# Kernel tuning notes

Measured on AMD Instinct MI355X. Metric: run time of the kernel, lower is better.

The kernel has to match this reference:

```python
import jax, jax.numpy as jnp
import numpy as np

B, IN_F, OUT_F = 1024, 256, 256
GRID_SIZE, K = 5, 3  # grid_size, spline_order
N_BASIS = GRID_SIZE + K


def _make_grid():
    h = (1.0 - (-1.0)) / GRID_SIZE
    return jnp.linspace(-1.0 - K * h, 1.0 + K * h, GRID_SIZE + 2 * K + 1, dtype=jnp.float32)


def compute_bspline_basis(x, grid, k):
    # x: (N,), grid: (G + 2k + 1,) -> (N, G + k)
    x = x[:, None]
    bases = ((x >= grid[:-1]) & (x < grid[1:])).astype(x.dtype)
    for p in range(1, k + 1):
        n = bases.shape[1] - 1
        left_den = jnp.clip(grid[p:p + n] - grid[:n], 1e-8)
        left = (x - grid[:n]) / left_den * bases[:, :n]
        right_den = jnp.clip(grid[p + 1:p + 1 + n] - grid[1:1 + n], 1e-8)
        right = (grid[p + 1:p + 1 + n] - x) / right_den * bases[:, 1:1 + n]
        bases = left + right
    # boundary fix: x at/above last interior knot falls into last basis
    bases = bases.at[:, -1].add((x[:, 0] >= grid[-k - 1]).astype(x.dtype))
    return bases


def setup_inputs() -> dict:
    key = jax.random.key(0)
    kx, kc, kb = jax.random.split(key, 3)
    x = jax.random.normal(kx, (B, IN_F), dtype=jnp.float32)
    coeff = jax.random.normal(kc, (OUT_F, IN_F, N_BASIS), dtype=jnp.float32) / np.sqrt(IN_F * N_BASIS)
    base_weight = jax.random.normal(kb, (OUT_F, IN_F), dtype=jnp.float32) / np.sqrt(IN_F)
    spline_weight = jnp.ones((OUT_F, IN_F), dtype=jnp.float32)
    grid = _make_grid()
    return {"x": x, "grid": grid, "coeff": coeff,
            "base_weight": base_weight, "spline_weight": spline_weight}


def reference(x, grid, coeff, base_weight, spline_weight):
    batch = x.shape[0]
    bases = compute_bspline_basis(x.reshape(-1), grid, K)          # (B*in, n_basis)
    bases = bases.reshape(batch, IN_F, N_BASIS)                     # (b, i, n)
    spline_out = jnp.einsum('bin,oin->boi', bases, coeff)           # (b, o, i)
    spline_out = spline_out * spline_weight[None, :, :]
    base_out = jax.nn.silu(x)[:, None, :] * base_weight[None, :, :]  # (b, o, i)
    return (spline_out + base_out).sum(axis=2)                      # (b, o)
```

## Files before the change

### kernel.cpp

```cpp
#include <hip/hip_runtime.h>
#include <hip/hip_bf16.h>

#define B_SZ   1024
#define IN_F   256
#define OUT_F  256
#define NB     9
#define KTOT   (IN_F * NB)
#define NGRID  12

typedef __attribute__((ext_vector_type(8))) short  bf16x8;
typedef __attribute__((ext_vector_type(16))) float f32x16;

__global__ __launch_bounds__(256) void kan_prep(
    const float* __restrict__ x,
    const float* __restrict__ grid,
    const float* __restrict__ coeff,
    const float* __restrict__ bw,
    const float* __restrict__ sw,
    __hip_bfloat16* __restrict__ phi,
    __hip_bfloat16* __restrict__ W) {
  if (blockIdx.x < (B_SZ * IN_F) / 256) {
    int idx = blockIdx.x * 256 + threadIdx.x;
    float g[NGRID];
#pragma unroll
    for (int j = 0; j < NGRID; ++j) g[j] = grid[j];
    float xv = x[idx];

    float bas[NGRID - 1];
#pragma unroll
    for (int j = 0; j < NGRID - 1; ++j)
      bas[j] = (xv >= g[j] && xv < g[j + 1]) ? 1.0f : 0.0f;

    float h = g[1] - g[0];
    float r1 = __builtin_amdgcn_rcpf(h);
    float rp[3] = { r1, 0.5f * r1, (1.0f / 3.0f) * r1 };

#pragma unroll
    for (int p = 1; p <= 3; ++p) {
      int n = NGRID - 1 - p;
      float inv = rp[p - 1];
#pragma unroll
      for (int j = 0; j < n; ++j) {
        bas[j] = ((xv - g[j]) * bas[j] + (g[p + 1 + j] - xv) * bas[j + 1]) * inv;
      }
    }
    bas[7] += (xv >= g[NGRID - 4]) ? 1.0f : 0.0f;
    float sil = xv / (1.0f + __expf(-xv));

    int b = idx >> 8;
    int i = idx & 255;
    __hip_bfloat16* dst = phi + (size_t)b * KTOT + i;
#pragma unroll
    for (int n = 0; n < 8; ++n) dst[n * IN_F] = __float2bfloat16(bas[n]);
    dst[8 * IN_F] = __float2bfloat16(sil);
  } else {
    int idx = (blockIdx.x - (B_SZ * IN_F) / 256) * 256 + threadIdx.x;
    int o = idx >> 8;
    int i = idx & 255;
    float s = sw[idx];
    const float4* c4 = (const float4*)(coeff + (size_t)idx * 8);
    float4 c0 = c4[0];
    float4 c1 = c4[1];
    __hip_bfloat16* dst = W + (size_t)o * KTOT + i;
    dst[0 * IN_F] = __float2bfloat16(s * c0.x);
    dst[1 * IN_F] = __float2bfloat16(s * c0.y);
    dst[2 * IN_F] = __float2bfloat16(s * c0.z);
    dst[3 * IN_F] = __float2bfloat16(s * c0.w);
    dst[4 * IN_F] = __float2bfloat16(s * c1.x);
    dst[5 * IN_F] = __float2bfloat16(s * c1.y);
    dst[6 * IN_F] = __float2bfloat16(s * c1.z);
    dst[7 * IN_F] = __float2bfloat16(s * c1.w);
    dst[8 * IN_F] = __float2bfloat16(bw[idx]);
  }
}

#define KSEG (KTOT / 16)

__global__ __launch_bounds__(1024) void kan_gemm(
    const __hip_bfloat16* __restrict__ phi,
    const __hip_bfloat16* __restrict__ W,
    float* __restrict__ out) {
  __shared__ float partial[8][32 * 32];

  int tid  = threadIdx.x;
  int wave = tid >> 6;
  int lane = tid & 63;
  int bm = (blockIdx.x & 31) * 32;
  int bn = (blockIdx.x >> 5) * 32;
  int r = lane & 31;
  int h = lane >> 5;

  const short* ap = (const short*)(phi + (size_t)(bm + r) * KTOT) + wave * KSEG + h * 8;
  const short* bp = (const short*)(W   + (size_t)(bn + r) * KTOT) + wave * KSEG + h * 8;

  f32x16 acc;
#pragma unroll
  for (int g = 0; g < 16; ++g) acc[g] = 0.0f;

#pragma unroll 3
  for (int k = 0; k < KSEG; k += 16) {
    bf16x8 a = *(const bf16x8*)(ap + k);
    bf16x8 b = *(const bf16x8*)(bp + k);
    acc = __builtin_amdgcn_mfma_f32_32x32x16_bf16(a, b, acc, 0, 0, 0);
  }

  float* pw = &partial[wave & 7][0];
  if (wave < 8) {
#pragma unroll
    for (int g = 0; g < 16; ++g) {
      int row = (g & 3) + 8 * (g >> 2) + 4 * h;
      pw[row * 32 + r] = acc[g];
    }
  }
  __syncthreads();
  if (wave >= 8) {
#pragma unroll
    for (int g = 0; g < 16; ++g) {
      int row = (g & 3) + 8 * (g >> 2) + 4 * h;
      pw[row * 32 + r] += acc[g];
    }
  }
  __syncthreads();

  float s = 0.0f;
#pragma unroll
  for (int w = 0; w < 8; ++w) s += partial[w][tid];
  int row = tid >> 5, col = tid & 31;
  out[(size_t)(bm + row) * OUT_F + bn + col] = s;
}

extern "C" void kernel_launch(void* const* d_in, const int* in_sizes, int n_in,
                              void* d_out, int out_size, void* d_ws, size_t ws_size,
                              hipStream_t stream) {
  const float* x     = (const float*)d_in[0];
  const float* grid  = (const float*)d_in[1];
  const float* coeff = (const float*)d_in[2];
  const float* bw    = (const float*)d_in[3];
  const float* sw    = (const float*)d_in[4];
  float* out = (float*)d_out;

  __hip_bfloat16* phi = (__hip_bfloat16*)d_ws;
  __hip_bfloat16* W   = phi + (size_t)B_SZ * KTOT;

  kan_prep<<<(B_SZ * IN_F + OUT_F * IN_F) / 256, 256, 0, stream>>>(
      x, grid, coeff, bw, sw, phi, W);
  kan_gemm<<<(B_SZ / 32) * (OUT_F / 32), 1024, 0, stream>>>(phi, W, out);
}
```

Baseline: 75.35 us.

## Fuse basis/weight preparation into GEMM kernel using LDS-staged tiles

Merges the prep and GEMM kernels into one launch. Each block computes B-spline bases and SiLU for its 32 batch rows and the scaled bf16 weights for its 32 outputs directly into shared memory, in two K-chunks, then runs MFMA over them with 12 waves. This removes the global workspace round trip and the second launch. In exchange, basis and weight work is recomputed redundantly across blocks, and LDS stores with a stride of 9 may cause bank conflicts.

Result: slower. 82.04 us (+8.9%).

```diff
diff --git a/kernel.cpp b/kernel.cpp
--- a/kernel.cpp
+++ b/kernel.cpp
@@ -8,125 +8,137 @@
 #define KTOT   (IN_F * NB)
 #define NGRID  12
 
+#define ICH    128
+#define KCH    (ICH * NB)
+#define STR    (KCH + 8)
+#define NWAVE  12
+#define THREADS 768
+#define KSEG   (KCH / NWAVE)
+
 typedef __attribute__((ext_vector_type(8))) short  bf16x8;
 typedef __attribute__((ext_vector_type(16))) float f32x16;
 
-__global__ __launch_bounds__(256) void kan_prep(
+__device__ __forceinline__ short f2bs(float v) {
+  __hip_bfloat16 b = __float2bfloat16(v);
+  return *reinterpret_cast<short*>(&b);
+}
+
+__global__ __launch_bounds__(THREADS) void kan_fused(
     const float* __restrict__ x,
     const float* __restrict__ grid,
     const float* __restrict__ coeff,
     const float* __restrict__ bw,
     const float* __restrict__ sw,
-    __hip_bfloat16* __restrict__ phi,
-    __hip_bfloat16* __restrict__ W) {
-  if (blockIdx.x < (B_SZ * IN_F) / 256) {
-    int idx = blockIdx.x * 256 + threadIdx.x;
-    float g[NGRID];
-#pragma unroll
-    for (int j = 0; j < NGRID; ++j) g[j] = grid[j];
-    float xv = x[idx];
-
-    float bas[NGRID - 1];
-#pragma unroll
-    for (int j = 0; j < NGRID - 1; ++j)
-      bas[j] = (xv >= g[j] && xv < g[j + 1]) ? 1.0f : 0.0f;
-
-    float h = g[1] - g[0];
-    float r1 = __builtin_amdgcn_rcpf(h);
-    float rp[3] = { r1, 0.5f * r1, (1.0f / 3.0f) * r1 };
-
-#pragma unroll
-    for (int p = 1; p <= 3; ++p) {
-      int n = NGRID - 1 - p;
-      float inv = rp[p - 1];
-#pragma unroll
-      for (int j = 0; j < n; ++j) {
-        bas[j] = ((xv - g[j]) * bas[j] + (g[p + 1 + j] - xv) * bas[j + 1]) * inv;
-      }
-    }
-    bas[7] += (xv >= g[NGRID - 4]) ? 1.0f : 0.0f;
-    float sil = xv / (1.0f + __expf(-xv));
-
-    int b = idx >> 8;
-    int i = idx & 255;
-    __hip_bfloat16* dst = phi + (size_t)b * KTOT + i;
-#pragma unroll
-    for (int n = 0; n < 8; ++n) dst[n * IN_F] = __float2bfloat16(bas[n]);
-    dst[8 * IN_F] = __float2bfloat16(sil);
-  } else {
-    int idx = (blockIdx.x - (B_SZ * IN_F) / 256) * 256 + threadIdx.x;
-    int o = idx >> 8;
-    int i = idx & 255;
-    float s = sw[idx];
-    const float4* c4 = (const float4*)(coeff + (size_t)idx * 8);
-    float4 c0 = c4[0];
-    float4 c1 = c4[1];
-    __hip_bfloat16* dst = W + (size_t)o * KTOT + i;
-    dst[0 * IN_F] = __float2bfloat16(s * c0.x);
-    dst[1 * IN_F] = __float2bfloat16(s * c0.y);
-    dst[2 * IN_F] = __float2bfloat16(s * c0.z);
-    dst[3 * IN_F] = __float2bfloat16(s * c0.w);
-    dst[4 * IN_F] = __float2bfloat16(s * c1.x);
-    dst[5 * IN_F] = __float2bfloat16(s * c1.y);
-    dst[6 * IN_F] = __float2bfloat16(s * c1.z);
-    dst[7 * IN_F] = __float2bfloat16(s * c1.w);
-    dst[8 * IN_F] = __float2bfloat16(bw[idx]);
-  }
-}
-
-#define KSEG (KTOT / 16)
-
-__global__ __launch_bounds__(1024) void kan_gemm(
-    const __hip_bfloat16* __restrict__ phi,
-    const __hip_bfloat16* __restrict__ W,
     float* __restrict__ out) {
-  __shared__ float partial[8][32 * 32];
+  __shared__ __align__(16) short smem[2 * 32 * STR];
+  short* As = smem;
+  short* Bs = smem + 32 * STR;
 
   int tid  = threadIdx.x;
   int wave = tid >> 6;
   int lane = tid & 63;
+  int r = lane & 31;
+  int h = lane >> 5;
   int bm = (blockIdx.x & 31) * 32;
   int bn = (blockIdx.x >> 5) * 32;
-  int r = lane & 31;
-  int h = lane >> 5;
 
-  const short* ap = (const short*)(phi + (size_t)(bm + r) * KTOT) + wave * KSEG + h * 8;
-  const short* bp = (const short*)(W   + (size_t)(bn + r) * KTOT) + wave * KSEG + h * 8;
+  float g[NGRID];
+#pragma unroll
+  for (int j = 0; j < NGRID; ++j) g[j] = grid[j];
+  float hh = g[1] - g[0];
+  float r1 = __builtin_amdgcn_rcpf(hh);
+  float rp[3] = { r1, 0.5f * r1, (1.0f / 3.0f) * r1 };
 
   f32x16 acc;
 #pragma unroll
-  for (int g = 0; g < 16; ++g) acc[g] = 0.0f;
+  for (int q = 0; q < 16; ++q) acc[q] = 0.0f;
 
-#pragma unroll 3
-  for (int k = 0; k < KSEG; k += 16) {
-    bf16x8 a = *(const bf16x8*)(ap + k);
-    bf16x8 b = *(const bf16x8*)(bp + k);
-    acc = __builtin_amdgcn_mfma_f32_32x32x16_bf16(a, b, acc, 0, 0, 0);
+  for (int c = 0; c < 2; ++c) {
+    int i0 = c * ICH;
+
+    for (int p = tid; p < 32 * ICH; p += THREADS) {
+      int row = p >> 7;
+      int i   = p & (ICH - 1);
+      float xv = x[(size_t)(bm + row) * IN_F + i0 + i];
+
+      float bas[NGRID - 1];
+#pragma unroll
+      for (int j = 0; j < NGRID - 1; ++j)
+        bas[j] = (xv >= g[j] && xv < g[j + 1]) ? 1.0f : 0.0f;
+#pragma unroll
+      for (int p3 = 1; p3 <= 3; ++p3) {
+        int n = NGRID - 1 - p3;
+        float inv = rp[p3 - 1];
+#pragma unroll
+        for (int j = 0; j < n; ++j)
+          bas[j] = ((xv - g[j]) * bas[j] + (g[p3 + 1 + j] - xv) * bas[j + 1]) * inv;
+      }
+      bas[7] += (xv >= g[NGRID - 4]) ? 1.0f : 0.0f;
+      float sil = xv / (1.0f + __expf(-xv));
+
+      short* d = As + row * STR + i * NB;
+#pragma unroll
+      for (int n = 0; n < 8; ++n) d[n] = f2bs(bas[n]);
+      d[8] = f2bs(sil);
+    }
+
+    for (int p = tid; p < 32 * ICH; p += THREADS) {
+      int o = p >> 7;
+      int i = p & (ICH - 1);
+      int gi = (bn + o) * IN_F + i0 + i;
+      float s = sw[gi];
+      const float4* c4 = (const float4*)(coeff + (size_t)gi * 8);
+      float4 c0 = c4[0];
+      float4 c1 = c4[1];
+      short* d = Bs + o * STR + i * NB;
+      d[0] = f2bs(s * c0.x);
+      d[1] = f2bs(s * c0.y);
+      d[2] = f2bs(s * c0.z);
+      d[3] = f2bs(s * c0.w);
+      d[4] = f2bs(s * c1.x);
+      d[5] = f2bs(s * c1.y);
+      d[6] = f2bs(s * c1.z);
+      d[7] = f2bs(s * c1.w);
+      d[8] = f2bs(bw[gi]);
+    }
+    __syncthreads();
+
+    const short* ap = As + r * STR + wave * KSEG + h * 8;
+    const short* bp = Bs + r * STR + wave * KSEG + h * 8;
+#pragma unroll
+    for (int k = 0; k < KSEG; k += 16) {
+      bf16x8 a = *(const bf16x8*)(ap + k);
+      bf16x8 b = *(const bf16x8*)(bp + k);
+      acc = __builtin_amdgcn_mfma_f32_32x32x16_bf16(a, b, acc, 0, 0, 0);
+    }
+    __syncthreads();
   }
 
-  float* pw = &partial[wave & 7][0];
-  if (wave < 8) {
+  float* partial = (float*)smem;
+  float* pw = partial + (wave % 6) * 1024;
+  if (wave < 6) {
 #pragma unroll
-    for (int g = 0; g < 16; ++g) {
-      int row = (g & 3) + 8 * (g >> 2) + 4 * h;
-      pw[row * 32 + r] = acc[g];
+    for (int q = 0; q < 16; ++q) {
+      int crow = (q & 3) + 8 * (q >> 2) + 4 * h;
+      pw[crow * 32 + r] = acc[q];
     }
   }
   __syncthreads();
-  if (wave >= 8) {
+  if (wave >= 6) {
 #pragma unroll
-    for (int g = 0; g < 16; ++g) {
-      int row = (g & 3) + 8 * (g >> 2) + 4 * h;
-      pw[row * 32 + r] += acc[g];
+    for (int q = 0; q < 16; ++q) {
+      int crow = (q & 3) + 8 * (q >> 2) + 4 * h;
+      pw[crow * 32 + r] += acc[q];
     }
   }
   __syncthreads();
 
-  float s = 0.0f;
+  for (int e = tid; e < 1024; e += THREADS) {
+    float s = 0.0f;
 #pragma unroll
-  for (int w = 0; w < 8; ++w) s += partial[w][tid];
-  int row = tid >> 5, col = tid & 31;
-  out[(size_t)(bm + row) * OUT_F + bn + col] = s;
+    for (int w = 0; w < 6; ++w) s += partial[w * 1024 + e];
+    out[(size_t)(bm + (e >> 5)) * OUT_F + bn + (e & 31)] = s;
+  }
 }
 
 extern "C" void kernel_launch(void* const* d_in, const int* in_sizes, int n_in,
@@ -138,11 +150,8 @@
   const float* bw    = (const float*)d_in[3];
   const float* sw    = (const float*)d_in[4];
   float* out = (float*)d_out;
+  (void)d_ws; (void)ws_size;
 
-  __hip_bfloat16* phi = (__hip_bfloat16*)d_ws;
-  __hip_bfloat16* W   = phi + (size_t)B_SZ * KTOT;
-
-  kan_prep<<<(B_SZ * IN_F + OUT_F * IN_F) / 256, 256, 0, stream>>>(
-      x, grid, coeff, bw, sw, phi, W);
-  kan_gemm<<<(B_SZ / 32) * (OUT_F / 32), 1024, 0, stream>>>(phi, W, out);
+  kan_fused<<<(B_SZ / 32) * (OUT_F / 32), THREADS, 0, stream>>>(
+      x, grid, coeff, bw, sw, out);
 }
```
